# Kernel tuning notes

Measured on AMD Instinct MI355X. Metric: run time of the kernel, lower is better.

Reference implementation:

```python
import jax, jax.numpy as jnp
import numpy as np

L, H, NH, DH, FF, V, S, B = 12, 768, 12, 64, 3072, 21128, 512, 8
SEP = 102
LN_EPS = 1e-12


def _ln(x, g, b):
    m = jnp.mean(x, axis=-1, keepdims=True)
    v = jnp.mean(jnp.square(x - m), axis=-1, keepdims=True)
    return (x - m) * jax.lax.rsqrt(v + LN_EPS) * g + b


def setup_inputs() -> dict:
    key = jax.random.key(0)
    ctr = [0]
    def nk():
        ctr[0] += 1
        return jax.random.fold_in(key, ctr[0])
    def p(shape):
        return (0.02 * jax.random.normal(nk(), shape)).astype(jnp.float32)

    input_ids = jax.random.randint(nk(), (B, S), 0, V)
    sep_cols = jax.random.randint(nk(), (B,), 32, 128)
    input_ids = input_ids.at[jnp.arange(B), sep_cols].set(SEP)  # plant [SEP] per row
    labels = jax.random.randint(nk(), (B, S), 0, V)

    return dict(
        input_ids=input_ids, labels=labels,
        word_emb=p((V, H)), pos_emb=p((S, H)), type_emb=p((2, H)),
        emb_ln_g=jnp.ones((H,), jnp.float32), emb_ln_b=jnp.zeros((H,), jnp.float32),
        Wq=p((L, H, H)), bq=jnp.zeros((L, H), jnp.float32),
        Wk=p((L, H, H)), bk=jnp.zeros((L, H), jnp.float32),
        Wv=p((L, H, H)), bv=jnp.zeros((L, H), jnp.float32),
        Wo=p((L, H, H)), bo=jnp.zeros((L, H), jnp.float32),
        ln1_g=jnp.ones((L, H), jnp.float32), ln1_b=jnp.zeros((L, H), jnp.float32),
        Wi=p((L, H, FF)), bi=jnp.zeros((L, FF), jnp.float32),
        Wd=p((L, FF, H)), bd=jnp.zeros((L, H), jnp.float32),
        ln2_g=jnp.ones((L, H), jnp.float32), ln2_b=jnp.zeros((L, H), jnp.float32),
        Wc=p((H, V)), bc=jnp.zeros((V,), jnp.float32),
    )


def reference(input_ids, labels, word_emb, pos_emb, type_emb, emb_ln_g, emb_ln_b,
              Wq, bq, Wk, bk, Wv, bv, Wo, bo, ln1_g, ln1_b,
              Wi, bi, Wd, bd, ln2_g, ln2_b, Wc, bc):
    Bn, Sn = input_ids.shape
    # UniLM prefix-causal mask: bidirectional up to (and incl.) first SEP, causal after
    eq = input_ids == SEP
    sep = jnp.where(eq.any(axis=1), jnp.argmax(eq, axis=1), Sn - 1)        # [B]
    qi = jnp.arange(Sn)[:, None]
    ki = jnp.arange(Sn)[None, :]
    causal = (ki <= qi)                                                    # [S,S]
    prefix = (qi[None] <= sep[:, None, None]) & (ki[None] <= sep[:, None, None])
    mask = (causal[None] | prefix).astype(jnp.float32)                     # [B,S,S]
    bias = ((1.0 - mask) * -1e4)[:, None]                                  # [B,1,S,S]

    # BERT embeddings (token_type all zeros)
    x = word_emb[input_ids] + pos_emb[None, :Sn] + type_emb[0]
    x = _ln(x, emb_ln_g, emb_ln_b)

    scale = 1.0 / np.sqrt(DH).astype(np.float32)
    for l in range(L):
        q = (x @ Wq[l] + bq[l]).reshape(Bn, Sn, NH, DH)
        k = (x @ Wk[l] + bk[l]).reshape(Bn, Sn, NH, DH)
        v = (x @ Wv[l] + bv[l]).reshape(Bn, Sn, NH, DH)
        scores = jnp.einsum('bqhd,bkhd->bhqk', q, k) * scale + bias        # [B,NH,S,S]
        probs = jax.nn.softmax(scores, axis=-1)
        ctx = jnp.einsum('bhqk,bkhd->bqhd', probs, v).reshape(Bn, Sn, H)
        x = _ln(x + ctx @ Wo[l] + bo[l], ln1_g[l], ln1_b[l])
        h = jax.nn.gelu(x @ Wi[l] + bi[l], approximate=False)
        x = _ln(x + h @ Wd[l] + bd[l], ln2_g[l], ln2_b[l])

    logits = x @ Wc + bc                                                   # [B,S,V]
    logp = jax.nn.log_softmax(logits, axis=-1)
    valid = labels >= 0                                                    # ignore_index=-100
    safe = jnp.where(valid, labels, 0)
    nll = -jnp.take_along_axis(logp, safe[..., None], axis=-1)[..., 0]
    loss = jnp.sum(nll * valid) / jnp.maximum(jnp.sum(valid), 1)
    return loss
```

## Files before the change

### kernel.cpp

```cpp
#include <hip/hip_runtime.h>
#include <hip/hip_bf16.h>
#include <cmath>

namespace {

constexpr int LAYERS = 12;
constexpr int H   = 768;
constexpr int NH  = 12;
constexpr int DH  = 64;
constexpr int FF  = 3072;
constexpr int V   = 21128;
constexpr int S   = 512;
constexpr int B   = 8;
constexpr int M   = B * S;
constexpr int SEP = 102;
constexpr int NPAD = 21248;
constexpr int NT64 = NPAD / 64;
constexpr int QKVN = 3 * H;
constexpr size_t MHc = (size_t)M * H;

typedef __attribute__((ext_vector_type(8))) short short8;
typedef __attribute__((ext_vector_type(4))) float floatx4;

__device__ __forceinline__ float geluf(float x) {
  return 0.5f * x * (1.0f + erff(x * 0.70710678118654752f));
}

__device__ __forceinline__ void gload16(const void* g, void* l) {
  __builtin_amdgcn_global_load_lds(
      (const __attribute__((address_space(1))) void*)g,
      (__attribute__((address_space(3))) void*)l, 16, 0, 0);
}

__device__ __forceinline__ unsigned short f2bf(float f) {
  __hip_bfloat16 h = __float2bfloat16(f);
  return *reinterpret_cast<unsigned short*>(&h);
}

__device__ __forceinline__ float block_sum256(float v, float* red) {
  int tid = threadIdx.x;
  red[tid] = v; __syncthreads();
  for (int s2 = 128; s2 > 0; s2 >>= 1) {
    if (tid < s2) red[tid] += red[tid + s2];
    __syncthreads();
  }
  float r = red[0];
  __syncthreads();
  return r;
}

__device__ __forceinline__ float block_max256(float v, float* red) {
  int tid = threadIdx.x;
  red[tid] = v; __syncthreads();
  for (int s2 = 128; s2 > 0; s2 >>= 1) {
    if (tid < s2) red[tid] = fmaxf(red[tid], red[tid + s2]);
    __syncthreads();
  }
  float r = red[0];
  __syncthreads();
  return r;
}

__global__ void sep_kernel(const int* __restrict__ ids, int* __restrict__ sep) {
  int b = blockIdx.x;
  __shared__ int red[256];
  int m = S - 1;
  for (int s = threadIdx.x; s < S; s += 256)
    if (ids[b * S + s] == SEP) m = min(m, s);
  red[threadIdx.x] = m; __syncthreads();
  for (int s2 = 128; s2 > 0; s2 >>= 1) {
    if (threadIdx.x < s2) red[threadIdx.x] = min(red[threadIdx.x], red[threadIdx.x + s2]);
    __syncthreads();
  }
  if (threadIdx.x == 0) sep[b] = red[0];
}

__global__ __launch_bounds__(256) void transpose_kernel(
    const float* __restrict__ W, __hip_bfloat16* __restrict__ Wt,
    int K, int N, int Npad, size_t in_stride, size_t out_stride) {
  const float* Wz = W + (size_t)blockIdx.z * in_stride;
  __hip_bfloat16* Wtz = Wt + (size_t)blockIdx.z * out_stride;
  __shared__ float tile[32][33];
  int k0 = blockIdx.x * 32, n0 = blockIdx.y * 32;
  int tx = threadIdx.x & 31, ty = threadIdx.x >> 5;
  #pragma unroll
  for (int i = 0; i < 4; i++) {
    int kk = k0 + ty + i * 8, nn = n0 + tx;
    tile[ty + i * 8][tx] = (kk < K && nn < N) ? Wz[(size_t)kk * N + nn] : 0.f;
  }
  __syncthreads();
  #pragma unroll
  for (int i = 0; i < 4; i++) {
    int nn = n0 + ty + i * 8, kk = k0 + tx;
    if (nn < Npad && kk < K)
      Wtz[(size_t)nn * K + kk] = __float2bfloat16(tile[tx][ty + i * 8]);
  }
}

__global__ __launch_bounds__(256) void embed_kernel(
    const int* __restrict__ ids, const float* __restrict__ we,
    const float* __restrict__ pe, const float* __restrict__ te,
    const float* __restrict__ g, const float* __restrict__ bta,
    float* __restrict__ x, __hip_bfloat16* __restrict__ xb) {
  __shared__ float red[256];
  int tok = blockIdx.x;
  int s = tok % S;
  int id = ids[tok];
  float vals[3];
  #pragma unroll
  for (int i = 0; i < 3; i++) {
    int hh = threadIdx.x + i * 256;
    vals[i] = we[(size_t)id * H + hh] + pe[(size_t)s * H + hh] + te[hh];
  }
  float mean = block_sum256(vals[0] + vals[1] + vals[2], red) * (1.0f / H);
  float sq = 0.f;
  #pragma unroll
  for (int i = 0; i < 3; i++) { float d = vals[i] - mean; sq += d * d; }
  float var = block_sum256(sq, red) * (1.0f / H);
  float inv = rsqrtf(var + 1e-12f);
  #pragma unroll
  for (int i = 0; i < 3; i++) {
    int hh = threadIdx.x + i * 256;
    float o = (vals[i] - mean) * inv * g[hh] + bta[hh];
    x[(size_t)tok * H + hh] = o;
    xb[(size_t)tok * H + hh] = __float2bfloat16(o);
  }
}

template <int NS>
__global__ __launch_bounds__(256) void add_ln_kernel(
    const float* __restrict__ resid, const float* __restrict__ t,
    const float* __restrict__ g, const float* __restrict__ bta,
    float* __restrict__ out, __hip_bfloat16* __restrict__ outb) {
  __shared__ float red[256];
  int tok = blockIdx.x;
  float vals[3];
  #pragma unroll
  for (int i = 0; i < 3; i++) {
    size_t idx = (size_t)tok * H + threadIdx.x + i * 256;
    float v = resid[idx];
    #pragma unroll
    for (int z = 0; z < NS; z++) v += t[z * MHc + idx];
    vals[i] = v;
  }
  float mean = block_sum256(vals[0] + vals[1] + vals[2], red) * (1.0f / H);
  float sq = 0.f;
  #pragma unroll
  for (int i = 0; i < 3; i++) { float d = vals[i] - mean; sq += d * d; }
  float var = block_sum256(sq, red) * (1.0f / H);
  float inv = rsqrtf(var + 1e-12f);
  #pragma unroll
  for (int i = 0; i < 3; i++) {
    int hh = threadIdx.x + i * 256;
    float o = (vals[i] - mean) * inv * g[hh] + bta[hh];
    out[(size_t)tok * H + hh] = o;
    outb[(size_t)tok * H + hh] = __float2bfloat16(o);
  }
}

template <int K, int N, int EPI, int SPLIT = 1, bool SWZ = false>
__global__ __launch_bounds__(256) void mfma_gemm(
    const short* __restrict__ A, const short* __restrict__ Bt,
    const float* __restrict__ bias,
    float* __restrict__ Cf, __hip_bfloat16* __restrict__ Cb,
    const int* __restrict__ labels, float2* __restrict__ partials,
    float* __restrict__ lablogit,
    __hip_bfloat16* __restrict__ Cb2, __hip_bfloat16* __restrict__ Cb3,
    const float* __restrict__ bias2, const float* __restrict__ bias3) {
  __shared__ __align__(16) short lds_a[128 * 64];
  __shared__ __align__(16) short lds_b[128 * 64];
  const int tid = threadIdx.x, lane = tid & 63, w = tid >> 6;
  const int wm = w >> 1, wn = w & 1;
  const int g = lane >> 4, c16 = lane & 15;

  int bx = blockIdx.x, by = blockIdx.y;
  if constexpr (SWZ) {
    constexpr int NBX = N / 128;
    constexpr int GR = M / 128;
    constexpr int NWG = NBX * GR;
    static_assert(NWG % 8 == 0, "swizzle needs nwg %% 8 == 0");
    int lid = by * NBX + bx;
    int j = (lid & 7) * (NWG >> 3) + (lid >> 3);
    bx = j / GR; by = j % GR;
  }
  const int row0 = by * 128, col0 = bx * 128;

  floatx4 acc[4][4] = {};

  constexpr int Ks = K / SPLIT;
  const int koff = (SPLIT > 1) ? (int)blockIdx.z * Ks : 0;

  for (int k0 = koff; k0 < koff + Ks; k0 += 64) {
    #pragma unroll
    for (int j = 0; j < 4; j++) {
      int row = w * 32 + j * 8 + (lane >> 3);
      int cg = (lane & 7) ^ (row & 7);
      gload16(A + (size_t)(row0 + row) * K + (k0 + cg * 8),
              lds_a + w * 2048 + j * 512 + lane * 8);
      gload16(Bt + (size_t)(col0 + row) * K + (k0 + cg * 8),
              lds_b + w * 2048 + j * 512 + lane * 8);
    }
    __syncthreads();
    #pragma unroll
    for (int ks = 0; ks < 2; ks++) {
      short8 af[4], bfr[4];
      #pragma unroll
      for (int t = 0; t < 4; t++) {
        int rm = wm * 64 + t * 16 + c16;
        af[t] = *(const short8*)(lds_a + rm * 64 + (((ks * 4 + g) ^ (rm & 7)) << 3));
        int rn = wn * 64 + t * 16 + c16;
        bfr[t] = *(const short8*)(lds_b + rn * 64 + (((ks * 4 + g) ^ (rn & 7)) << 3));
      }
      #pragma unroll
      for (int mt = 0; mt < 4; mt++)
        #pragma unroll
        for (int nt = 0; nt < 4; nt++)
          acc[mt][nt] = __builtin_amdgcn_mfma_f32_16x16x32_bf16(af[mt], bfr[nt], acc[mt][nt], 0, 0, 0);
    }
    __syncthreads();
  }

  if constexpr (EPI == 0) {
    float* Cfz = Cf + (size_t)blockIdx.z * ((size_t)M * N);
    #pragma unroll
    for (int mt = 0; mt < 4; mt++)
      #pragma unroll
      for (int r = 0; r < 4; r++) {
        int row = row0 + wm * 64 + mt * 16 + g * 4 + r;
        #pragma unroll
        for (int nt = 0; nt < 4; nt++) {
          int col = col0 + wn * 64 + nt * 16 + c16;
          float bb = (SPLIT == 1 || blockIdx.z == 0) ? bias[col] : 0.f;
          Cfz[(size_t)row * N + col] = acc[mt][nt][r] + bb;
        }
      }
  } else if constexpr (EPI == 1 || EPI == 2) {
    #pragma unroll
    for (int mt = 0; mt < 4; mt++)
      #pragma unroll
      for (int r = 0; r < 4; r++) {
        int row = row0 + wm * 64 + mt * 16 + g * 4 + r;
        #pragma unroll
        for (int nt = 0; nt < 4; nt++) {
          int col = col0 + wn * 64 + nt * 16 + c16;
          float vv = acc[mt][nt][r] + bias[col];
          if constexpr (EPI == 2) vv = geluf(vv);
          Cb[(size_t)row * N + col] = __float2bfloat16(vv);
        }
      }
  } else if constexpr (EPI == 5) {
    const int sect = col0 / H;
    const int lc0 = col0 - sect * H;
    if (sect < 2) {
      __hip_bfloat16* out = (sect == 0) ? Cb : Cb2;
      const float* bptr = (sect == 0) ? bias : bias2;
      #pragma unroll
      for (int mt = 0; mt < 4; mt++)
        #pragma unroll
        for (int r = 0; r < 4; r++) {
          int row = row0 + wm * 64 + mt * 16 + g * 4 + r;
          #pragma unroll
          for (int nt = 0; nt < 4; nt++) {
            int lc = lc0 + wn * 64 + nt * 16 + c16;
            out[(size_t)row * H + lc] = __float2bfloat16(acc[mt][nt][r] + bptr[lc]);
          }
        }
    } else {
      unsigned short* vt = (unsigned short*)Cb3;
      #pragma unroll
      for (int mt = 0; mt < 4; mt++) {
        int row = row0 + wm * 64 + mt * 16 + g * 4;
        int bb = row >> 9, s0 = row & 511;
        #pragma unroll
        for (int nt = 0; nt < 4; nt++) {
          int lc = lc0 + wn * 64 + nt * 16 + c16;
          int h = lc >> 6, d = lc & 63;
          float bcol = bias3[lc];
          uint2 u;
          unsigned short p0 = f2bf(acc[mt][nt][0] + bcol);
          unsigned short p1 = f2bf(acc[mt][nt][1] + bcol);
          unsigned short p2 = f2bf(acc[mt][nt][2] + bcol);
          unsigned short p3 = f2bf(acc[mt][nt][3] + bcol);
          u.x = (unsigned int)p0 | ((unsigned int)p1 << 16);
          u.y = (unsigned int)p2 | ((unsigned int)p3 << 16);
          *(uint2*)(vt + ((size_t)((bb * NH + h) * DH + d) << 9) + s0) = u;
        }
      }
    }
  } else {
    #pragma unroll
    for (int mt = 0; mt < 4; mt++)
      #pragma unroll
      for (int r = 0; r < 4; r++) {
        int row = row0 + wm * 64 + mt * 16 + g * 4 + r;
        int lab = labels[row];
        float vals[4];
        float rmax = -1e30f;
        #pragma unroll
        for (int nt = 0; nt < 4; nt++) {
          int col = col0 + wn * 64 + nt * 16 + c16;
          float vv = (col < V) ? (acc[mt][nt][r] + bias[col]) : -60000.0f;
          vals[nt] = vv;
          rmax = fmaxf(rmax, vv);
          if (col == lab) lablogit[row] = vv;
        }
        #pragma unroll
        for (int d = 1; d < 16; d <<= 1) rmax = fmaxf(rmax, __shfl_xor(rmax, d, 64));
        float se = 0.f;
        #pragma unroll
        for (int nt = 0; nt < 4; nt++) se += __expf(vals[nt] - rmax);
        #pragma unroll
        for (int d = 1; d < 16; d <<= 1) se += __shfl_xor(se, d, 64);
        if (c16 == 0)
          partials[(size_t)row * NT64 + (col0 >> 6) + wn] = make_float2(rmax, se);
      }
  }
}

__global__ __launch_bounds__(256) void flash_attn(
    const short* __restrict__ q, const short* __restrict__ k,
    const short* __restrict__ vt, const int* __restrict__ sep,
    __hip_bfloat16* __restrict__ ctx) {
  constexpr int KT = 128;
  __shared__ __align__(16) short Qs[64 * 64];
  __shared__ __align__(16) short Ks[128 * 64];
  __shared__ __align__(16) short Vts[64 * 128];
  __shared__ __align__(16) short Pb[64 * 136];
  __shared__ __align__(16) float wm4[4][64];
  __shared__ __align__(16) float wl4[4][64];
  __shared__ __align__(16) float m_run[64], l_run[64], alpha_s[64], mnew_s[64];

  const int tid = threadIdx.x, lane = tid & 63, w = tid >> 6;
  const int g = lane >> 4, c16 = lane & 15;
  const int qt0 = blockIdx.x * 64, h = blockIdx.y, b = blockIdx.z;
  const int sepb = sep[b];

  if (tid < 64) { m_run[tid] = -1e30f; l_run[tid] = 0.f; }

  #pragma unroll
  for (int t = 0; t < 2; t++) {
    int id = (w * 2 + t) * 64 + lane;
    int row = id >> 3, slot = id & 7;
    int c = slot ^ (row & 7);
    gload16(q + (size_t)(b * S + qt0 + row) * H + h * DH + c * 8,
            Qs + (w * 2 + t) * 512);
  }

  int niter = (qt0 + 64 + KT - 1) / KT;
  int sepit = (sepb >> 7) + 1;
  if (sepit > niter) niter = sepit;

  floatx4 accO[4] = {};
  short8 qf[4][2];

  for (int it = 0; it < niter; ++it) {
    int kk0 = it * KT;
    __syncthreads();
    #pragma unroll
    for (int t = 0; t < 4; t++) {
      int id = (w * 4 + t) * 64 + lane;
      {
        int row = id >> 3, slot = id & 7, c = slot ^ (row & 7);
        gload16(k + (size_t)(b * S + kk0 + row) * H + h * DH + c * 8,
                Ks + (w * 4 + t) * 512);
      }
      {
        int row = id >> 4, slot = id & 15, c = slot ^ (row & 15);
        gload16(vt + (size_t)((b * NH + h) * DH + row) * S + kk0 + c * 8,
                Vts + (w * 4 + t) * 512);
      }
    }
    __syncthreads();

    if (it == 0) {
      #pragma unroll
      for (int nt = 0; nt < 4; nt++)
        #pragma unroll
        for (int st = 0; st < 2; st++) {
          int qq = nt * 16 + c16;
          int slot = (st * 4 + g) ^ (qq & 7);
          qf[nt][st] = *(const short8*)(Qs + qq * 64 + slot * 8);
        }
    }

    floatx4 accS[2][4] = {};
    #pragma unroll
    for (int st = 0; st < 2; st++) {
      short8 af[2];
      #pragma unroll
      for (int mt = 0; mt < 2; mt++) {
        int kkr = w * 32 + mt * 16 + c16;
        int slot = (st * 4 + g) ^ (kkr & 7);
        af[mt] = *(const short8*)(Ks + kkr * 64 + slot * 8);
      }
      #pragma unroll
      for (int mt = 0; mt < 2; mt++)
        #pragma unroll
        for (int nt = 0; nt < 4; nt++)
          accS[mt][nt] = __builtin_amdgcn_mfma_f32_16x16x32_bf16(
              af[mt], qf[nt][st], accS[mt][nt], 0, 0, 0);
    }

    float sc[2][4][4];
    float pm[4] = {-1e30f, -1e30f, -1e30f, -1e30f};
    #pragma unroll
    for (int mt = 0; mt < 2; mt++)
      #pragma unroll
      for (int nt = 0; nt < 4; nt++)
        #pragma unroll
        for (int r = 0; r < 4; r++) {
          int kkg = kk0 + w * 32 + mt * 16 + g * 4 + r;
          int qg = qt0 + nt * 16 + c16;
          bool allowed = (kkg <= qg) || (qg <= sepb && kkg <= sepb);
          float vv = accS[mt][nt][r] * 0.125f + (allowed ? 0.f : -1e4f);
          sc[mt][nt][r] = vv;
          pm[nt] = fmaxf(pm[nt], vv);
        }
    #pragma unroll
    for (int nt = 0; nt < 4; nt++) {
      pm[nt] = fmaxf(pm[nt], __shfl_xor(pm[nt], 16, 64));
      pm[nt] = fmaxf(pm[nt], __shfl_xor(pm[nt], 32, 64));
    }
    if (lane < 16) {
      #pragma unroll
      for (int nt = 0; nt < 4; nt++) wm4[w][nt * 16 + c16] = pm[nt];
    }
    __syncthreads();
    if (tid < 64) {
      float mit = fmaxf(fmaxf(wm4[0][tid], wm4[1][tid]), fmaxf(wm4[2][tid], wm4[3][tid]));
      float mold = m_run[tid];
      float mnew = fmaxf(mold, mit);
      float al = __expf(mold - mnew);
      m_run[tid] = mnew;
      alpha_s[tid] = al;
      mnew_s[tid] = mnew;
      l_run[tid] *= al;
    }
    __syncthreads();

    float psum[4] = {};
    #pragma unroll
    for (int mt = 0; mt < 2; mt++)
      #pragma unroll
      for (int nt = 0; nt < 4; nt++) {
        int qg = nt * 16 + c16;
        float mn = mnew_s[qg];
        unsigned short pk[4];
        #pragma unroll
        for (int r = 0; r < 4; r++) {
          float p = __expf(sc[mt][nt][r] - mn);
          psum[nt] += p;
          pk[r] = f2bf(p);
        }
        int kb = w * 32 + mt * 16 + g * 4;
        uint2 u;
        u.x = (unsigned int)pk[0] | ((unsigned int)pk[1] << 16);
        u.y = (unsigned int)pk[2] | ((unsigned int)pk[3] << 16);
        *(uint2*)(Pb + qg * 136 + kb) = u;
      }
    #pragma unroll
    for (int nt = 0; nt < 4; nt++) {
      psum[nt] += __shfl_xor(psum[nt], 16, 64);
      psum[nt] += __shfl_xor(psum[nt], 32, 64);
    }
    if (lane < 16) {
      #pragma unroll
      for (int nt = 0; nt < 4; nt++) wl4[w][nt * 16 + c16] = psum[nt];
    }
    {
      float4 a4 = *(const float4*)(alpha_s + w * 16 + g * 4);
      #pragma unroll
      for (int nt = 0; nt < 4; nt++) {
        accO[nt][0] *= a4.x; accO[nt][1] *= a4.y;
        accO[nt][2] *= a4.z; accO[nt][3] *= a4.w;
      }
    }
    __syncthreads();
    if (tid < 64)
      l_run[tid] += wl4[0][tid] + wl4[1][tid] + wl4[2][tid] + wl4[3][tid];

    #pragma unroll
    for (int st = 0; st < 4; st++) {
      short8 pf = *(const short8*)(Pb + (w * 16 + c16) * 136 + st * 32 + g * 8);
      #pragma unroll
      for (int nt = 0; nt < 4; nt++) {
        int d = nt * 16 + c16;
        int slot = (st * 4 + g) ^ (d & 15);
        short8 vf = *(const short8*)(Vts + d * 128 + slot * 8);
        accO[nt] = __builtin_amdgcn_mfma_f32_16x16x32_bf16(pf, vf, accO[nt], 0, 0, 0);
      }
    }
  }

  __syncthreads();
  float4 lv = *(const float4*)(l_run + w * 16 + g * 4);
  float linv[4] = {1.0f / lv.x, 1.0f / lv.y, 1.0f / lv.z, 1.0f / lv.w};
  #pragma unroll
  for (int r = 0; r < 4; r++) {
    int row = b * S + qt0 + w * 16 + g * 4 + r;
    #pragma unroll
    for (int nt = 0; nt < 4; nt++)
      ctx[(size_t)row * H + h * DH + nt * 16 + c16] =
          __float2bfloat16(accO[nt][r] * linv[r]);
  }
}

__global__ __launch_bounds__(256) void loss_kernel(
    const float2* __restrict__ partials, const float* __restrict__ lablogit,
    const int* __restrict__ labels, float* __restrict__ acc) {
  int tok = blockIdx.x;
  if (labels[tok] < 0) return;
  __shared__ float red[256];
  float lm = -1e30f;
  for (int t = threadIdx.x; t < NT64; t += 256)
    lm = fmaxf(lm, partials[(size_t)tok * NT64 + t].x);
  float Mx = block_max256(lm, red);
  float ls = 0.f;
  for (int t = threadIdx.x; t < NT64; t += 256) {
    float2 p = partials[(size_t)tok * NT64 + t];
    ls += p.y * __expf(p.x - Mx);
  }
  float Ssum = block_sum256(ls, red);
  if (threadIdx.x == 0) {
    float nll = (Mx + logf(Ssum)) - lablogit[tok];
    atomicAdd(&acc[0], nll);
    atomicAdd(&acc[1], 1.0f);
  }
}

__global__ void finalize_kernel(const float* __restrict__ acc, float* __restrict__ out) {
  out[0] = acc[0] / fmaxf(acc[1], 1.0f);
}

}

extern "C" void kernel_launch(void* const* d_in, const int* in_sizes, int n_in,
                              void* d_out, int out_size, void* d_ws, size_t ws_size,
                              hipStream_t stream) {
  const int*   input_ids = (const int*)d_in[0];
  const int*   labels    = (const int*)d_in[1];
  const float* word_emb  = (const float*)d_in[2];
  const float* pos_emb   = (const float*)d_in[3];
  const float* type_emb  = (const float*)d_in[4];
  const float* emb_ln_g  = (const float*)d_in[5];
  const float* emb_ln_b  = (const float*)d_in[6];
  const float* Wq = (const float*)d_in[7];
  const float* bq = (const float*)d_in[8];
  const float* Wk = (const float*)d_in[9];
  const float* bk = (const float*)d_in[10];
  const float* Wv = (const float*)d_in[11];
  const float* bv = (const float*)d_in[12];
  const float* Wo = (const float*)d_in[13];
  const float* bo = (const float*)d_in[14];
  const float* ln1_g = (const float*)d_in[15];
  const float* ln1_b = (const float*)d_in[16];
  const float* Wi = (const float*)d_in[17];
  const float* bi = (const float*)d_in[18];
  const float* Wd = (const float*)d_in[19];
  const float* bd = (const float*)d_in[20];
  const float* ln2_g = (const float*)d_in[21];
  const float* ln2_b = (const float*)d_in[22];
  const float* Wc = (const float*)d_in[23];
  const float* bc = (const float*)d_in[24];

  char* base = (char*)d_ws;
  size_t off = 0;
  auto alloc = [&](size_t bytes) -> void* {
    void* p = base + off;
    off = (off + bytes + 255) & ~(size_t)255;
    return p;
  };
  const size_t MH = (size_t)M * H;
  float*          x        = (float*)alloc(MH * 4);
  float*          t2       = (float*)alloc(MH * 4 * 4);
  __hip_bfloat16* xb       = (__hip_bfloat16*)alloc(MH * 2);
  __hip_bfloat16* qb       = (__hip_bfloat16*)alloc(MH * 2);
  __hip_bfloat16* kb       = (__hip_bfloat16*)alloc(MH * 2);
  __hip_bfloat16* vt       = (__hip_bfloat16*)alloc((size_t)B * NH * DH * S * 2);
  __hip_bfloat16* ctxb     = (__hip_bfloat16*)alloc(MH * 2);
  __hip_bfloat16* t1b      = (__hip_bfloat16*)alloc((size_t)M * FF * 2);
  float2*         partials = (float2*)alloc((size_t)M * NT64 * 8);
  float*          lablogit = (float*)alloc((size_t)M * 4);
  float*          acc      = (float*)alloc(2 * 4);
  int*            sep      = (int*)alloc(B * 4);
  __hip_bfloat16* wqkv_t = (__hip_bfloat16*)alloc((size_t)LAYERS * QKVN * H * 2);
  __hip_bfloat16* wo_t = (__hip_bfloat16*)alloc((size_t)LAYERS * H * H * 2);
  __hip_bfloat16* wi_t = (__hip_bfloat16*)alloc((size_t)FF * H * 2);
  __hip_bfloat16* wd_t = (__hip_bfloat16*)alloc((size_t)H * FF * 2);
  __hip_bfloat16* wc_t = (__hip_bfloat16*)alloc((size_t)NPAD * H * 2);

  hipMemsetAsync(acc, 0, 2 * sizeof(float), stream);

  sep_kernel<<<B, 256, 0, stream>>>(input_ids, sep);
  embed_kernel<<<M, 256, 0, stream>>>(input_ids, word_emb, pos_emb, type_emb,
                                      emb_ln_g, emb_ln_b, x, xb);

  {
    dim3 tg(H / 32, H / 32, LAYERS);
    transpose_kernel<<<tg, 256, 0, stream>>>(Wq, wqkv_t, H, H, H,
                                             (size_t)H * H, (size_t)QKVN * H);
    transpose_kernel<<<tg, 256, 0, stream>>>(Wk, wqkv_t + (size_t)H * H, H, H, H,
                                             (size_t)H * H, (size_t)QKVN * H);
    transpose_kernel<<<tg, 256, 0, stream>>>(Wv, wqkv_t + (size_t)2 * H * H, H, H, H,
                                             (size_t)H * H, (size_t)QKVN * H);
    transpose_kernel<<<tg, 256, 0, stream>>>(Wo, wo_t, H, H, H, (size_t)H * H, (size_t)H * H);
    dim3 tgc(H / 32, NPAD / 32, 1);
    transpose_kernel<<<tgc, 256, 0, stream>>>(Wc, wc_t, H, V, NPAD, 0, 0);
  }

  dim3 gQKV(QKVN / 128, M / 128);
  dim3 gO(H / 128, M / 128, 2);
  dim3 gF(FF / 128, M / 128);
  dim3 gD(H / 128, M / 128, 4);
  dim3 gAttn(S / 64, NH, B);

  for (int l = 0; l < LAYERS; l++) {
    transpose_kernel<<<dim3(H / 32, FF / 32, 1), 256, 0, stream>>>(
        Wi + (size_t)l * H * FF, wi_t, H, FF, FF, 0, 0);
    transpose_kernel<<<dim3(FF / 32, H / 32, 1), 256, 0, stream>>>(
        Wd + (size_t)l * FF * H, wd_t, FF, H, H, 0, 0);

    const short* xbs = (const short*)xb;
    mfma_gemm<H, QKVN, 5><<<gQKV, 256, 0, stream>>>(
        xbs, (const short*)(wqkv_t + (size_t)l * QKVN * H), bq + (size_t)l * H,
        nullptr, qb, nullptr, nullptr, nullptr,
        kb, vt, bk + (size_t)l * H, bv + (size_t)l * H);
    flash_attn<<<gAttn, 256, 0, stream>>>(
        (const short*)qb, (const short*)kb, (const short*)vt, sep, ctxb);
    mfma_gemm<H, H, 0, 2><<<gO, 256, 0, stream>>>(
        (const short*)ctxb, (const short*)(wo_t + (size_t)l * H * H), bo + (size_t)l * H,
        t2, nullptr, nullptr, nullptr, nullptr,
        nullptr, nullptr, nullptr, nullptr);
    add_ln_kernel<2><<<M, 256, 0, stream>>>(x, t2, ln1_g + (size_t)l * H,
                                            ln1_b + (size_t)l * H, x, xb);
    mfma_gemm<H, FF, 2><<<gF, 256, 0, stream>>>(
        (const short*)xb, (const short*)wi_t, bi + (size_t)l * FF,
        nullptr, t1b, nullptr, nullptr, nullptr,
        nullptr, nullptr, nullptr, nullptr);
    mfma_gemm<FF, H, 0, 4><<<gD, 256, 0, stream>>>(
        (const short*)t1b, (const short*)wd_t, bd + (size_t)l * H,
        t2, nullptr, nullptr, nullptr, nullptr,
        nullptr, nullptr, nullptr, nullptr);
    add_ln_kernel<4><<<M, 256, 0, stream>>>(x, t2, ln2_g + (size_t)l * H,
                                            ln2_b + (size_t)l * H, x, xb);
  }

  dim3 gV(NPAD / 128, M / 128);
  mfma_gemm<H, NPAD, 3, 1, true><<<gV, 256, 0, stream>>>(
      (const short*)xb, (const short*)wc_t, bc,
      nullptr, nullptr, labels, partials, lablogit,
      nullptr, nullptr, nullptr, nullptr);
  loss_kernel<<<M, 256, 0, stream>>>(partials, lablogit, labels, acc);
  finalize_kernel<<<1, 1, 0, stream>>>(acc, (float*)d_out);
}
```

Before: 3.417 ms.

## Double-buffer GEMM LDS tiles with K=32 steps to overlap loads and MFMA

The main MFMA GEMM loop changes from a single 64-wide K tile with two barriers per step to two 32-wide K buffers in LDS. The next tile's global-to-LDS load is issued before computing on the current one, with one barrier per iteration. The LDS swizzle is redone for the 32-element row layout. The aim is to hide global load latency behind MFMA work. In exchange, each barrier now covers half as much compute and the new swizzle may cause different LDS bank conflicts.

```diff
diff --git a/kernel.cpp b/kernel.cpp
--- a/kernel.cpp
+++ b/kernel.cpp
@@ -167,11 +167,13 @@
     float* __restrict__ lablogit,
     __hip_bfloat16* __restrict__ Cb2, __hip_bfloat16* __restrict__ Cb3,
     const float* __restrict__ bias2, const float* __restrict__ bias3) {
-  __shared__ __align__(16) short lds_a[128 * 64];
-  __shared__ __align__(16) short lds_b[128 * 64];
+  __shared__ __align__(16) short lds_a[2][128 * 32];
+  __shared__ __align__(16) short lds_b[2][128 * 32];
   const int tid = threadIdx.x, lane = tid & 63, w = tid >> 6;
   const int wm = w >> 1, wn = w & 1;
   const int g = lane >> 4, c16 = lane & 15;
+  const int srow = w * 32 + (lane >> 2);
+  const int schunk = lane & 3;
 
   int bx = blockIdx.x, by = blockIdx.y;
   if constexpr (SWZ) {
@@ -188,35 +190,41 @@
   floatx4 acc[4][4] = {};
 
   constexpr int Ks = K / SPLIT;
+  constexpr int NTK = Ks / 32;
   const int koff = (SPLIT > 1) ? (int)blockIdx.z * Ks : 0;
 
-  for (int k0 = koff; k0 < koff + Ks; k0 += 64) {
-    #pragma unroll
-    for (int j = 0; j < 4; j++) {
-      int row = w * 32 + j * 8 + (lane >> 3);
-      int cg = (lane & 7) ^ (row & 7);
-      gload16(A + (size_t)(row0 + row) * K + (k0 + cg * 8),
-              lds_a + w * 2048 + j * 512 + lane * 8);
-      gload16(Bt + (size_t)(col0 + row) * K + (k0 + cg * 8),
-              lds_b + w * 2048 + j * 512 + lane * 8);
-    }
-    __syncthreads();
-    #pragma unroll
-    for (int ks = 0; ks < 2; ks++) {
-      short8 af[4], bfr[4];
-      #pragma unroll
-      for (int t = 0; t < 4; t++) {
-        int rm = wm * 64 + t * 16 + c16;
-        af[t] = *(const short8*)(lds_a + rm * 64 + (((ks * 4 + g) ^ (rm & 7)) << 3));
-        int rn = wn * 64 + t * 16 + c16;
-        bfr[t] = *(const short8*)(lds_b + rn * 64 + (((ks * 4 + g) ^ (rn & 7)) << 3));
-      }
-      #pragma unroll
-      for (int mt = 0; mt < 4; mt++)
-        #pragma unroll
-        for (int nt = 0; nt < 4; nt++)
-          acc[mt][nt] = __builtin_amdgcn_mfma_f32_16x16x32_bf16(af[mt], bfr[nt], acc[mt][nt], 0, 0, 0);
-    }
+  auto stage = [&](int buf, int k0) {
+    #pragma unroll
+    for (int j = 0; j < 2; j++) {
+      int m = srow + j * 16;
+      int cg = schunk ^ ((m >> 1) & 3);
+      gload16(A + (size_t)(row0 + m) * K + (k0 + cg * 8),
+              &lds_a[buf][w * 1024 + j * 512]);
+      gload16(Bt + (size_t)(col0 + m) * K + (k0 + cg * 8),
+              &lds_b[buf][w * 1024 + j * 512]);
+    }
+  };
+
+  stage(0, koff);
+  __syncthreads();
+
+  #pragma unroll 2
+  for (int t = 0; t < NTK; ++t) {
+    const int cur = t & 1;
+    if (t + 1 < NTK) stage(cur ^ 1, koff + (t + 1) * 32);
+    short8 af[4], bfr[4];
+    #pragma unroll
+    for (int tt = 0; tt < 4; tt++) {
+      int rm = wm * 64 + tt * 16 + c16;
+      af[tt] = *(const short8*)(&lds_a[cur][rm * 32 + ((g ^ ((rm >> 1) & 3)) << 3)]);
+      int rn = wn * 64 + tt * 16 + c16;
+      bfr[tt] = *(const short8*)(&lds_b[cur][rn * 32 + ((g ^ ((rn >> 1) & 3)) << 3)]);
+    }
+    #pragma unroll
+    for (int mt = 0; mt < 4; mt++)
+      #pragma unroll
+      for (int nt = 0; nt < 4; nt++)
+        acc[mt][nt] = __builtin_amdgcn_mfma_f32_16x16x32_bf16(af[mt], bfr[nt], acc[mt][nt], 0, 0, 0);
     __syncthreads();
   }
 
```

Measured after the change: 3.498 ms. +2.4%, slower.
